# Optimization experiments

Measured on AMD Instinct MI355X. Metric: run time of the kernel, lower is better.

The kernel has to match this reference:

```python
import jax, jax.numpy as jnp
import numpy as np

B, C, P, E, M, H, K = 1024, 8192, 3, 64, 128, 16, 8
SCALE = 0.05
EPS = 1e-12  # tf.math.l2_normalize epsilon


def setup_inputs() -> dict:
    key = jax.random.key(0)
    ks = jax.random.split(key, 16)
    return {
        'pools': jax.random.uniform(ks[0], (B, C), dtype=jnp.float32),            # dense stand-in for SparseTensor batch_pools
        'metapaths': jax.random.uniform(ks[1], (P, C, C), dtype=jnp.float32),     # card-card metapath matrices
        'card_embeddings': jax.random.normal(ks[2], (C, E), dtype=jnp.float32) * SCALE,
        'mp_kernels': jax.random.normal(ks[3], (P, E, M), dtype=jnp.float32) * SCALE,
        'mp_biases': jnp.zeros((P, M, 1), dtype=jnp.float32),
        'Wq': jax.random.normal(ks[4], (M, H, K), dtype=jnp.float32) * SCALE,
        'bq': jnp.zeros((H, K), dtype=jnp.float32),
        'Wk': jax.random.normal(ks[5], (M, H, K), dtype=jnp.float32) * SCALE,
        'bk': jnp.zeros((H, K), dtype=jnp.float32),
        'Wv': jax.random.normal(ks[6], (M, H, K), dtype=jnp.float32) * SCALE,
        'bv': jnp.zeros((H, K), dtype=jnp.float32),
        'Wo': jax.random.normal(ks[7], (H, K, M), dtype=jnp.float32) * SCALE,
        'bo': jnp.zeros((M,), dtype=jnp.float32),
        'pool_kernel': jax.random.normal(ks[8], (M, E), dtype=jnp.float32) * SCALE,
        'pool_bias': jnp.zeros((E,), dtype=jnp.float32),
    }


def _l2_normalize(x, axis):
    # matches tf.math.l2_normalize: x / sqrt(max(sum(x^2), eps))
    sq = jnp.sum(jnp.square(x), axis=axis, keepdims=True)
    return x * jax.lax.rsqrt(jnp.maximum(sq, EPS))


def reference(pools, metapaths, card_embeddings, mp_kernels, mp_biases,
              Wq, bq, Wk, bk, Wv, bv, Wo, bo, pool_kernel, pool_bias):
    # --- MetapathEmbed layers, vectorized over the P metapaths ---
    # path_card_embeddings: act(einsum('ce,em->mc') + bias) -> (P, M, C)
    path_card = jax.nn.silu(jnp.einsum('ce,pem->pmc', card_embeddings, mp_kernels) + mp_biases)
    # path_card_matrix: einsum('mc,cd->dm') -> (P, C, M)
    pcm = jnp.einsum('pmc,pcd->pdm', path_card, metapaths)
    # sparse_dense_matmul(batch_pools, path_card_matrix); stack over metapaths -> (B, P, M)
    x = jnp.einsum('bd,pdm->bpm', pools, pcm)

    # --- keras MultiHeadAttention(query=x, value=x) ---
    q = jnp.einsum('bpm,mhk->bphk', x, Wq) + bq
    k = jnp.einsum('bpm,mhk->bphk', x, Wk) + bk
    v = jnp.einsum('bpm,mhk->bphk', x, Wv) + bv
    scores = jnp.einsum('bphk,bqhk->bhpq', q, k) / np.float32(np.sqrt(K))
    attn = jax.nn.softmax(scores, axis=-1)
    o = jnp.einsum('bhpq,bqhk->bphk', attn, v)
    attended = jnp.einsum('bphk,hkm->bpm', o, Wo) + bo  # (B, P, M)

    # --- pooling head ---
    pre_pool = jnp.sum(attended, axis=1)                       # (B, M)
    pool_embeds = jnp.einsum('bm,me->be', pre_pool, pool_kernel) + pool_bias
    norm_pool = _l2_normalize(pool_embeds, axis=1)             # (B, E)
    norm_cards = _l2_normalize(card_embeddings, axis=1)        # (C, E)
    return (jnp.einsum('be,ce->bc', norm_pool, norm_cards) + 1.0) / 2.0
```

## Files before the change

kernel.cpp:

```cpp
#include <hip/hip_runtime.h>

typedef unsigned int uint;
typedef unsigned short ushort;
typedef float f32x4 __attribute__((ext_vector_type(4)));
typedef short s16x8 __attribute__((ext_vector_type(8)));
typedef int i32x4 __attribute__((ext_vector_type(4)));
typedef uint u32x2 __attribute__((ext_vector_type(2)));

#define C_DIM 8192
#define B_DIM 1024
#define P_DIM 3
#define E_DIM 64
#define M_DIM 128

#define PCA_OFF   0ull
#define PART_OFF  15728640ull
#define PCMH_OFF  40894464ull
#define PCML_OFF  47185920ull
#define XPART_OFF PART_OFF
#define NPOOL_OFF 53477376ull
#define NCARD_OFF 53608448ull

__device__ __forceinline__ uint bf16_rne(float f) {
  uint u = __builtin_bit_cast(uint, f);
  return (u + 0x7fffu + ((u >> 16) & 1u)) >> 16;
}
__device__ __forceinline__ float bf16_to_f32(uint b) {
  return __builtin_bit_cast(float, b << 16);
}
__device__ __forceinline__ void glds16(const void* gsrc, void* ldst) {
  __builtin_amdgcn_global_load_lds(
      (const __attribute__((address_space(1))) uint*)gsrc,
      (__attribute__((address_space(3))) uint*)ldst, 16, 0, 0);
}

__global__ __launch_bounds__(256) void k1_pathcard(
    const float* __restrict__ cardemb, const float* __restrict__ mpk,
    const float* __restrict__ mpbias, ushort* __restrict__ pcA) {
  __shared__ float ce_l[64 * 68];
  const int tid = threadIdx.x;
  const int cb = blockIdx.x;
  const int p  = blockIdx.y;
  for (int r = 0; r < 16; ++r) {
    int i = r * 256 + tid;
    int row = i >> 6, col = i & 63;
    ce_l[row * 68 + col] = cardemb[(size_t)(cb * 64 + row) * 64 + col];
  }
  __syncthreads();
  const int m = tid & 127;
  const int chalf = tid >> 7;
  float kr[64];
#pragma unroll
  for (int e = 0; e < 64; ++e) kr[e] = mpk[(size_t)p * E_DIM * M_DIM + e * M_DIM + m];
  const float bias = mpbias[p * M_DIM + m];
  for (int cl0 = 0; cl0 < 32; ++cl0) {
    int cl = chalf * 32 + cl0;
    float acc = bias;
#pragma unroll
    for (int e = 0; e < 64; ++e) acc += ce_l[cl * 68 + e] * kr[e];
    float s = acc / (1.0f + expf(-acc));
    uint hb = bf16_rne(s);
    uint lb = bf16_rne(s - bf16_to_f32(hb));
    int c = cb * 64 + cl;
    int kt = c >> 5, kl = c & 31;
    size_t off = ((size_t)(p * 256 + kt) * 20480 + (size_t)m * 80 + (size_t)kl * 2) >> 1;
    pcA[off] = (ushort)hb;
    pcA[off + 5120] = (ushort)lb;
  }
}

__global__ __launch_bounds__(256, 2) void k2_big(
    const float* __restrict__ mp, const ushort* __restrict__ pcA,
    float* __restrict__ partial) {
  extern __shared__ char smem[];
  const int tid = threadIdx.x;
  const int dt = blockIdx.x, q = blockIdx.y, p = blockIdx.z;
  const int lane = tid & 63, wid = tid >> 6;
  const int wr = wid >> 1, wc = wid & 1;
  const int r16 = lane & 15, g4 = lane >> 4;
  const float* mpb = mp + (size_t)p * C_DIM * C_DIM + (size_t)dt * 128;
  const char* pcb = (const char*)pcA + (size_t)(p * 256 + q * 128) * 20480;
  const int sd = tid & 127, skh = tid >> 7;

  f32x4 acc[4][4];
#pragma unroll
  for (int i = 0; i < 4; ++i)
#pragma unroll
    for (int j = 0; j < 4; ++j) acc[i][j] = (f32x4){0.f, 0.f, 0.f, 0.f};

  auto stageA = [&](int t, int buf) {
    const char* src = pcb + (size_t)t * 20480;
    char* dst = smem + buf * 20480;
#pragma unroll
    for (int r = 0; r < 5; ++r)
      glds16(src + r * 4096 + wid * 1024 + lane * 16, dst + r * 4096 + wid * 1024);
  };
  auto loadB = [&](int t, float* br) {
    int c0 = q * 4096 + t * 32;
#pragma unroll
    for (int ii = 0; ii < 2; ++ii) {
      const float* rp = mpb + (size_t)(c0 + ii * 16 + skh * 8) * C_DIM + sd;
#pragma unroll
      for (int j = 0; j < 8; ++j) br[ii * 8 + j] = rp[(size_t)j * C_DIM];
    }
  };
  auto writeB = [&](const float* br) {
    char* bb = smem + 40960;
#pragma unroll
    for (int ii = 0; ii < 2; ++ii) {
      uint hw[4], lw[4];
#pragma unroll
      for (int k2 = 0; k2 < 4; ++k2) {
        float v0 = br[ii * 8 + k2 * 2], v1 = br[ii * 8 + k2 * 2 + 1];
        uint h0 = bf16_rne(v0), h1 = bf16_rne(v1);
        uint l0 = bf16_rne(v0 - bf16_to_f32(h0));
        uint l1 = bf16_rne(v1 - bf16_to_f32(h1));
        hw[k2] = h0 | (h1 << 16);
        lw[k2] = l0 | (l1 << 16);
      }
      int off = sd * 80 + ii * 32 + skh * 16;
      *(i32x4*)(bb + off) = (i32x4){(int)hw[0], (int)hw[1], (int)hw[2], (int)hw[3]};
      *(i32x4*)(bb + 10240 + off) = (i32x4){(int)lw[0], (int)lw[1], (int)lw[2], (int)lw[3]};
    }
  };
  auto compute = [&](int abuf) {
    const char* Ab = smem + abuf * 20480;
    const char* Bb = smem + 40960;
    s16x8 ah[4], al[4], bh[4], bl[4];
#pragma unroll
    for (int i = 0; i < 4; ++i) {
      int off = (wr * 64 + i * 16 + r16) * 80 + g4 * 16;
      ah[i] = *(const s16x8*)(Ab + off);
      al[i] = *(const s16x8*)(Ab + 10240 + off);
    }
#pragma unroll
    for (int j = 0; j < 4; ++j) {
      int off = (wc * 64 + j * 16 + r16) * 80 + g4 * 16;
      bh[j] = *(const s16x8*)(Bb + off);
      bl[j] = *(const s16x8*)(Bb + 10240 + off);
    }
#pragma unroll
    for (int i = 0; i < 4; ++i)
#pragma unroll
      for (int j = 0; j < 4; ++j) {
        acc[i][j] = __builtin_amdgcn_mfma_f32_16x16x32_bf16(ah[i], bh[j], acc[i][j], 0, 0, 0);
        acc[i][j] = __builtin_amdgcn_mfma_f32_16x16x32_bf16(ah[i], bl[j], acc[i][j], 0, 0, 0);
        acc[i][j] = __builtin_amdgcn_mfma_f32_16x16x32_bf16(al[i], bh[j], acc[i][j], 0, 0, 0);
      }
  };

  {
    float br[16];
    stageA(0, 0);
    loadB(0, br);
    writeB(br);
  }
  __syncthreads();
  for (int t = 0; t < 128; ++t) {
    int cur = t & 1;
    float brn[16];
    if (t < 127) {
      stageA(t + 1, cur ^ 1);
      loadB(t + 1, brn);
    }
    compute(cur);
    __syncthreads();
    if (t < 127) writeB(brn);
    __syncthreads();
  }
  float* part = partial + (size_t)(q * 3 + p) * M_DIM * C_DIM + (size_t)dt * 128;
#pragma unroll
  for (int i = 0; i < 4; ++i)
#pragma unroll
    for (int j = 0; j < 4; ++j)
#pragma unroll
      for (int r = 0; r < 4; ++r)
        part[(size_t)(wr * 64 + i * 16 + g4 * 4 + r) * C_DIM + (wc * 64 + j * 16 + r16)] =
            acc[i][j][r];
}

__global__ __launch_bounds__(256) void k2b_reduce(const float* __restrict__ p0,
                                                  ushort* __restrict__ oh,
                                                  ushort* __restrict__ ol) {
  size_t i = (size_t)blockIdx.x * 256 + threadIdx.x;
  f32x4 a = *(const f32x4*)(p0 + i * 4);
  f32x4 b = *(const f32x4*)(p0 + 3145728 + i * 4);
  f32x4 s = a + b;
  uint h[4], l[4];
#pragma unroll
  for (int k = 0; k < 4; ++k) {
    h[k] = bf16_rne(s[k]);
    l[k] = bf16_rne(s[k] - bf16_to_f32(h[k]));
  }
  *(u32x2*)(oh + i * 4) = (u32x2){h[0] | (h[1] << 16), h[2] | (h[3] << 16)};
  *(u32x2*)(ol + i * 4) = (u32x2){l[0] | (l[1] << 16), l[2] | (l[3] << 16)};
}

__global__ __launch_bounds__(256, 2) void k3_x(const float* __restrict__ pools,
                                               const ushort* __restrict__ pcmh,
                                               const ushort* __restrict__ pcml,
                                               float* __restrict__ xpart) {
  const int tid = threadIdx.x;
  const int bt = blockIdx.x, ks = blockIdx.y, p = blockIdx.z;
  const int lane = tid & 63, wid = tid >> 6;
  const int wr = wid >> 1, wc = wid & 1;
  const int r16 = lane & 15, g4 = lane >> 4;
  f32x4 acc[4][4];
#pragma unroll
  for (int i = 0; i < 4; ++i)
#pragma unroll
    for (int j = 0; j < 4; ++j) acc[i][j] = (f32x4){0.f, 0.f, 0.f, 0.f};

  for (int t = 0; t < 16; ++t) {
    int d0 = ks * 512 + t * 32 + g4 * 8;
    s16x8 ah[4], al[4], bh[4], bl[4];
#pragma unroll
    for (int i = 0; i < 4; ++i) {
      int row = bt * 128 + wr * 64 + i * 16 + r16;
      const float* ap = pools + (size_t)row * C_DIM + d0;
      f32x4 v0 = *(const f32x4*)ap;
      f32x4 v1 = *(const f32x4*)(ap + 4);
#pragma unroll
      for (int k = 0; k < 8; ++k) {
        float v = (k < 4) ? v0[k] : v1[k - 4];
        uint hb = bf16_rne(v);
        uint lb = bf16_rne(v - bf16_to_f32(hb));
        ah[i][k] = (short)hb;
        al[i][k] = (short)lb;
      }
    }
#pragma unroll
    for (int j = 0; j < 4; ++j) {
      int col = wc * 64 + j * 16 + r16;
      size_t boff = (size_t)(p * M_DIM + col) * C_DIM + d0;
      bh[j] = *(const s16x8*)(pcmh + boff);
      bl[j] = *(const s16x8*)(pcml + boff);
    }
#pragma unroll
    for (int i = 0; i < 4; ++i)
#pragma unroll
      for (int j = 0; j < 4; ++j) {
        acc[i][j] = __builtin_amdgcn_mfma_f32_16x16x32_bf16(ah[i], bh[j], acc[i][j], 0, 0, 0);
        acc[i][j] = __builtin_amdgcn_mfma_f32_16x16x32_bf16(ah[i], bl[j], acc[i][j], 0, 0, 0);
        acc[i][j] = __builtin_amdgcn_mfma_f32_16x16x32_bf16(al[i], bh[j], acc[i][j], 0, 0, 0);
      }
  }
#pragma unroll
  for (int i = 0; i < 4; ++i)
#pragma unroll
    for (int j = 0; j < 4; ++j)
#pragma unroll
      for (int r = 0; r < 4; ++r) {
        int row = bt * 128 + wr * 64 + i * 16 + g4 * 4 + r;
        xpart[((size_t)(ks * B_DIM + row) * 3 + p) * M_DIM + wc * 64 + j * 16 + r16] =
            acc[i][j][r];
      }
}

__global__ __launch_bounds__(128) void k4_attn(
    const float* __restrict__ xpart, const float* __restrict__ Wq,
    const float* __restrict__ bq, const float* __restrict__ Wk,
    const float* __restrict__ bk, const float* __restrict__ Wv,
    const float* __restrict__ bv, const float* __restrict__ Wo,
    const float* __restrict__ bo, const float* __restrict__ pk,
    const float* __restrict__ pb, ushort* __restrict__ npool) {
  __shared__ float xs[3 * 128], qa[3 * 128], ka[3 * 128], va[3 * 128], oa[3 * 128], pp[128];
  const int t = threadIdx.x;
  const int b = blockIdx.x;
#pragma unroll
  for (int p = 0; p < 3; ++p) {
    float v = 0.f;
    for (int ks = 0; ks < 16; ++ks)
      v += xpart[((size_t)(ks * B_DIM + b) * 3 + p) * M_DIM + t];
    xs[p * 128 + t] = v;
  }
  __syncthreads();
  float qv[3], kv[3], vv[3];
#pragma unroll
  for (int p = 0; p < 3; ++p) { qv[p] = bq[t]; kv[p] = bk[t]; vv[p] = bv[t]; }
  for (int m = 0; m < 128; ++m) {
    float wq = Wq[m * 128 + t], wk = Wk[m * 128 + t], wv = Wv[m * 128 + t];
#pragma unroll
    for (int p = 0; p < 3; ++p) {
      float xv = xs[p * 128 + m];
      qv[p] += xv * wq;
      kv[p] += xv * wk;
      vv[p] += xv * wv;
    }
  }
#pragma unroll
  for (int p = 0; p < 3; ++p) {
    qa[p * 128 + t] = qv[p];
    ka[p * 128 + t] = kv[p];
    va[p * 128 + t] = vv[p];
  }
  __syncthreads();
  const int h = t >> 3;
  float w[3][3];
#pragma unroll
  for (int p = 0; p < 3; ++p) {
    float s[3];
#pragma unroll
    for (int qq = 0; qq < 3; ++qq) {
      float d = 0.f;
#pragma unroll
      for (int kk = 0; kk < 8; ++kk)
        d += qa[p * 128 + h * 8 + kk] * ka[qq * 128 + h * 8 + kk];
      s[qq] = d / 2.8284271247461903f;
    }
    float mx = fmaxf(s[0], fmaxf(s[1], s[2]));
    float e0 = expf(s[0] - mx), e1 = expf(s[1] - mx), e2 = expf(s[2] - mx);
    float inv = 1.0f / (e0 + e1 + e2);
    w[p][0] = e0 * inv; w[p][1] = e1 * inv; w[p][2] = e2 * inv;
  }
#pragma unroll
  for (int p = 0; p < 3; ++p) {
    float o = w[p][0] * va[0 * 128 + t] + w[p][1] * va[1 * 128 + t] + w[p][2] * va[2 * 128 + t];
    oa[p * 128 + t] = o;
  }
  __syncthreads();
  float pre = 3.0f * bo[t];
#pragma unroll
  for (int p = 0; p < 3; ++p)
    for (int hk = 0; hk < 128; ++hk) pre += oa[p * 128 + hk] * Wo[hk * 128 + t];
  pp[t] = pre;
  __syncthreads();
  if (t < 64) {
    float pe = pb[t];
    for (int m = 0; m < 128; ++m) pe += pp[m] * pk[m * 64 + t];
    float ss = pe * pe;
#pragma unroll
    for (int off = 32; off; off >>= 1) ss += __shfl_xor(ss, off, 64);
    float rs = 1.0f / sqrtf(fmaxf(ss, 1e-12f));
    npool[b * 64 + t] = (ushort)bf16_rne(pe * rs);
  }
}

__global__ __launch_bounds__(256) void k4b_ncard(const float* __restrict__ ce,
                                                 ushort* __restrict__ ncard) {
  const int t = threadIdx.x;
  const int r = blockIdx.x * 4 + (t >> 6);
  const int lane = t & 63;
  float v = ce[(size_t)r * 64 + lane];
  float ss = v * v;
#pragma unroll
  for (int off = 32; off; off >>= 1) ss += __shfl_xor(ss, off, 64);
  float rs = 1.0f / sqrtf(fmaxf(ss, 1e-12f));
  ncard[(size_t)r * 64 + lane] = (ushort)bf16_rne(v * rs);
}

__global__ __launch_bounds__(256, 2) void k5_out(const ushort* __restrict__ np_,
                                                 const ushort* __restrict__ nc,
                                                 float* __restrict__ out) {
  const int tid = threadIdx.x;
  const int bt = blockIdx.x, ct = blockIdx.y;
  const int lane = tid & 63, wid = tid >> 6;
  const int wr = wid >> 1, wc = wid & 1;
  const int r16 = lane & 15, g4 = lane >> 4;
  f32x4 acc[4][4];
#pragma unroll
  for (int i = 0; i < 4; ++i)
#pragma unroll
    for (int j = 0; j < 4; ++j) acc[i][j] = (f32x4){0.f, 0.f, 0.f, 0.f};
#pragma unroll
  for (int ks = 0; ks < 2; ++ks) {
    int e0 = ks * 32 + g4 * 8;
    s16x8 af[4], bf_[4];
#pragma unroll
    for (int i = 0; i < 4; ++i)
      af[i] = *(const s16x8*)(np_ + (size_t)(bt * 128 + wr * 64 + i * 16 + r16) * 64 + e0);
#pragma unroll
    for (int j = 0; j < 4; ++j)
      bf_[j] = *(const s16x8*)(nc + (size_t)(ct * 128 + wc * 64 + j * 16 + r16) * 64 + e0);
#pragma unroll
    for (int i = 0; i < 4; ++i)
#pragma unroll
      for (int j = 0; j < 4; ++j)
        acc[i][j] = __builtin_amdgcn_mfma_f32_16x16x32_bf16(af[i], bf_[j], acc[i][j], 0, 0, 0);
  }
#pragma unroll
  for (int i = 0; i < 4; ++i)
#pragma unroll
    for (int j = 0; j < 4; ++j)
#pragma unroll
      for (int r = 0; r < 4; ++r) {
        int row = bt * 128 + wr * 64 + i * 16 + g4 * 4 + r;
        int col = ct * 128 + wc * 64 + j * 16 + r16;
        out[(size_t)row * C_DIM + col] = (acc[i][j][r] + 1.0f) * 0.5f;
      }
}

extern "C" void kernel_launch(void* const* d_in, const int* in_sizes, int n_in,
                              void* d_out, int out_size, void* d_ws, size_t ws_size,
                              hipStream_t stream) {
  const float* pools = (const float*)d_in[0];
  const float* metapaths = (const float*)d_in[1];
  const float* cardemb = (const float*)d_in[2];
  const float* mpk = (const float*)d_in[3];
  const float* mpbias = (const float*)d_in[4];
  const float* Wq = (const float*)d_in[5];
  const float* bq = (const float*)d_in[6];
  const float* Wk = (const float*)d_in[7];
  const float* bk = (const float*)d_in[8];
  const float* Wv = (const float*)d_in[9];
  const float* bv = (const float*)d_in[10];
  const float* Wo = (const float*)d_in[11];
  const float* bo = (const float*)d_in[12];
  const float* pk = (const float*)d_in[13];
  const float* pb = (const float*)d_in[14];
  float* out = (float*)d_out;
  char* ws = (char*)d_ws;

  ushort* pcA = (ushort*)(ws + PCA_OFF);
  float* part = (float*)(ws + PART_OFF);
  ushort* pcmh = (ushort*)(ws + PCMH_OFF);
  ushort* pcml = (ushort*)(ws + PCML_OFF);
  float* xpart = (float*)(ws + XPART_OFF);
  ushort* npool = (ushort*)(ws + NPOOL_OFF);
  ushort* ncard = (ushort*)(ws + NCARD_OFF);

  k1_pathcard<<<dim3(128, 3), dim3(256), 0, stream>>>(cardemb, mpk, mpbias, pcA);
  k2_big<<<dim3(64, 2, 3), dim3(256), 61440, stream>>>(metapaths, pcA, part);
  k2b_reduce<<<dim3(3072), dim3(256), 0, stream>>>(part, pcmh, pcml);
  k3_x<<<dim3(8, 16, 3), dim3(256), 0, stream>>>(pools, pcmh, pcml, xpart);
  k4b_ncard<<<dim3(2048), dim3(256), 0, stream>>>(cardemb, ncard);
  k4_attn<<<dim3(1024), dim3(128), 0, stream>>>(xpart, Wq, bq, Wk, bk, Wv, bv, Wo, bo, pk, pb,
                                                npool);
  k5_out<<<dim3(8, 64), dim3(256), 0, stream>>>(npool, ncard, out);
}
```

Measured before the change: 396.6 us.

## Pack bf16 splits with hardware cvt and deepen B prefetch in metapath GEMM

Replaces the manual bit-twiddling bf16 round-to-nearest-even with the packed __float22bfloat162_rn conversion, which on this hardware can map to a packed convert instruction. This applies to the hi/lo split in the metapath GEMM B staging, the reduce kernel and the pools conversion in k3. The main GEMM loop is also restructured: B register loads are issued two tiles ahead using ping-pong register buffers, and __syncthreads is replaced with explicit waitcnt and s_barrier so global loads stay in flight across barriers. This costs more registers and relies on hand-counted vmcnt values, which could break correctness or occupancy if the counts are wrong.

```diff
diff --git a/kernel.cpp b/kernel.cpp
--- a/kernel.cpp
+++ b/kernel.cpp
@@ -1,4 +1,5 @@
 #include <hip/hip_runtime.h>
+#include <hip/hip_bf16.h>
 
 typedef unsigned int uint;
 typedef unsigned short ushort;
@@ -27,6 +28,13 @@
 }
 __device__ __forceinline__ float bf16_to_f32(uint b) {
   return __builtin_bit_cast(float, b << 16);
+}
+__device__ __forceinline__ uint pk2(float a, float b) {
+  float2 t; t.x = a; t.y = b;
+  __hip_bfloat162 h2 = __float22bfloat162_rn(t);
+  uint r;
+  __builtin_memcpy(&r, &h2, 4);
+  return r;
 }
 __device__ __forceinline__ void glds16(const void* gsrc, void* ldst) {
   __builtin_amdgcn_global_load_lds(
@@ -112,11 +120,11 @@
 #pragma unroll
       for (int k2 = 0; k2 < 4; ++k2) {
         float v0 = br[ii * 8 + k2 * 2], v1 = br[ii * 8 + k2 * 2 + 1];
-        uint h0 = bf16_rne(v0), h1 = bf16_rne(v1);
-        uint l0 = bf16_rne(v0 - bf16_to_f32(h0));
-        uint l1 = bf16_rne(v1 - bf16_to_f32(h1));
-        hw[k2] = h0 | (h1 << 16);
-        lw[k2] = l0 | (l1 << 16);
+        uint h = pk2(v0, v1);
+        float h0 = __builtin_bit_cast(float, h << 16);
+        float h1 = __builtin_bit_cast(float, h & 0xffff0000u);
+        hw[k2] = h;
+        lw[k2] = pk2(v0 - h0, v1 - h1);
       }
       int off = sd * 80 + ii * 32 + skh * 16;
       *(i32x4*)(bb + off) = (i32x4){(int)hw[0], (int)hw[1], (int)hw[2], (int)hw[3]};
@@ -149,25 +157,37 @@
       }
   };
 
-  {
-    float br[16];
-    stageA(0, 0);
-    loadB(0, br);
-    writeB(br);
-  }
-  __syncthreads();
-  for (int t = 0; t < 128; ++t) {
-    int cur = t & 1;
-    float brn[16];
-    if (t < 127) {
-      stageA(t + 1, cur ^ 1);
-      loadB(t + 1, brn);
-    }
-    compute(cur);
-    __syncthreads();
-    if (t < 127) writeB(brn);
-    __syncthreads();
-  }
+  float brA[16], brB[16];
+  stageA(0, 0);
+  loadB(0, brA);
+  loadB(1, brB);
+  writeB(brA);
+  asm volatile("s_waitcnt lgkmcnt(0)" ::: "memory");
+  __builtin_amdgcn_s_barrier();
+
+#define K2_STEP(T, BUFC, BRW, BRL, TAIL)                                      \
+  {                                                                           \
+    int tn = (T) + 1 < 128 ? (T) + 1 : 127;                                   \
+    int tnn = (T) + 2 < 128 ? (T) + 2 : 127;                                  \
+    stageA(tn, 1 - (BUFC));                                                   \
+    loadB(tnn, BRL);                                                          \
+    compute(BUFC);                                                            \
+    __builtin_amdgcn_s_barrier();                                             \
+    if (!(TAIL)) {                                                            \
+      writeB(BRW);                                                            \
+      asm volatile("s_waitcnt lgkmcnt(0)" ::: "memory");                      \
+      asm volatile("s_waitcnt vmcnt(16)" ::: "memory");                       \
+      __builtin_amdgcn_s_barrier();                                           \
+    }                                                                         \
+  }
+
+  for (int t2 = 0; t2 < 64; ++t2) {
+    int t = 2 * t2;
+    K2_STEP(t, 0, brB, brA, false);
+    K2_STEP(t + 1, 1, brA, brB, (t2 == 63));
+  }
+#undef K2_STEP
+
   float* part = partial + (size_t)(q * 3 + p) * M_DIM * C_DIM + (size_t)dt * 128;
 #pragma unroll
   for (int i = 0; i < 4; ++i)
@@ -186,14 +206,18 @@
   f32x4 a = *(const f32x4*)(p0 + i * 4);
   f32x4 b = *(const f32x4*)(p0 + 3145728 + i * 4);
   f32x4 s = a + b;
-  uint h[4], l[4];
-#pragma unroll
-  for (int k = 0; k < 4; ++k) {
-    h[k] = bf16_rne(s[k]);
-    l[k] = bf16_rne(s[k] - bf16_to_f32(h[k]));
-  }
-  *(u32x2*)(oh + i * 4) = (u32x2){h[0] | (h[1] << 16), h[2] | (h[3] << 16)};
-  *(u32x2*)(ol + i * 4) = (u32x2){l[0] | (l[1] << 16), l[2] | (l[3] << 16)};
+  uint h[2], l[2];
+#pragma unroll
+  for (int k = 0; k < 2; ++k) {
+    float v0 = s[k * 2], v1 = s[k * 2 + 1];
+    uint hh = pk2(v0, v1);
+    float h0 = __builtin_bit_cast(float, hh << 16);
+    float h1 = __builtin_bit_cast(float, hh & 0xffff0000u);
+    h[k] = hh;
+    l[k] = pk2(v0 - h0, v1 - h1);
+  }
+  *(u32x2*)(oh + i * 4) = (u32x2){h[0], h[1]};
+  *(u32x2*)(ol + i * 4) = (u32x2){l[0], l[1]};
 }
 
 __global__ __launch_bounds__(256, 2) void k3_x(const float* __restrict__ pools,
@@ -220,14 +244,19 @@
       const float* ap = pools + (size_t)row * C_DIM + d0;
       f32x4 v0 = *(const f32x4*)ap;
       f32x4 v1 = *(const f32x4*)(ap + 4);
-#pragma unroll
-      for (int k = 0; k < 8; ++k) {
-        float v = (k < 4) ? v0[k] : v1[k - 4];
-        uint hb = bf16_rne(v);
-        uint lb = bf16_rne(v - bf16_to_f32(hb));
-        ah[i][k] = (short)hb;
-        al[i][k] = (short)lb;
-      }
+      i32x4 hw, lw;
+#pragma unroll
+      for (int k2 = 0; k2 < 4; ++k2) {
+        float a0 = (k2 < 2) ? v0[k2 * 2] : v1[(k2 - 2) * 2];
+        float a1 = (k2 < 2) ? v0[k2 * 2 + 1] : v1[(k2 - 2) * 2 + 1];
+        uint h = pk2(a0, a1);
+        float h0 = __builtin_bit_cast(float, h << 16);
+        float h1 = __builtin_bit_cast(float, h & 0xffff0000u);
+        hw[k2] = (int)h;
+        lw[k2] = (int)pk2(a0 - h0, a1 - h1);
+      }
+      ah[i] = __builtin_bit_cast(s16x8, hw);
+      al[i] = __builtin_bit_cast(s16x8, lw);
     }
 #pragma unroll
     for (int j = 0; j < 4; ++j) {
```

Measured after the change: 401.1 us. No clear change (+1.1%).
